# Performance work log

Hardware: AMD Instinct MI355X
Metric: run time of the kernel (lower is better)

Reference implementation:

```python
import math
import jax, jax.numpy as jnp
import numpy as np

B, N, M, H = 2, 4096, 32, 8
FDIM, LDIM, HID = 256, 10, 16
D = FDIM // H  # head_dim = 32


def setup_inputs() -> dict:
    key = jax.random.key(0)
    ks = jax.random.split(key, 16)
    rn = lambda i, shape, scale=1.0: jax.random.normal(ks[i], shape, jnp.float32) * scale
    return {
        "nbhd_pairwise_g": rn(0, (B, N, M, LDIM)),
        "nbhd_mask": jax.random.bernoulli(ks[1], 0.9, (B, N, M)),
        "key_features": rn(2, (B, N, FDIM)),
        "query_features": rn(3, (B, N, FDIM)),
        "nbhd_idx": jax.random.randint(ks[4], (B, N, M), 0, N, dtype=jnp.int32),
        # fc_k / fc_q (Linear feature_dim -> embed_dim)
        "Wk": rn(5, (FDIM, FDIM), 1.0 / math.sqrt(FDIM)),
        "bk": rn(6, (FDIM,), 0.01),
        "Wq": rn(7, (FDIM, FDIM), 1.0 / math.sqrt(FDIM)),
        "bq": rn(8, (FDIM,), 0.01),
        "W0": rn(9, (H, LDIM, HID), 1.0 / math.sqrt(LDIM)),
        "b0": rn(10, (H, HID), 0.01),
        "W1": rn(11, (H, HID, HID), 1.0 / math.sqrt(HID)),
        "b1": rn(12, (H, HID), 0.01),
        "W2": rn(13, (H, HID, 1), 1.0 / math.sqrt(HID)),
        "b2": rn(14, (H, 1), 0.01),
    }


def reference(nbhd_pairwise_g, nbhd_mask, key_features, query_features, nbhd_idx,
              Wk, bk, Wq, bq, W0, b0, W1, b1, W2, b2):
    # --- DotProductKernel: project, gather keys at nbhd_idx, scaled dot ---
    K = (key_features @ Wk + bk).reshape(B, N, H, D)      # (b,n,h,d)
    Q = (query_features @ Wq + bq).reshape(B, N, H, D)    # (b,n,h,d)
    # gather neighbor keys: Kn[b,i,j] = K[b, nbhd_idx[b,i,j]]  -> (b,n,m,h,d)
    Kn = K[jnp.arange(B)[:, None, None], nbhd_idx]
    # same math as full QK^T followed by A_[B,NNS,nbhd_idx], without the n x n matrix
    feat = jnp.einsum('bnhd,bnmhd->bnmh', Q, Kn) / math.sqrt(D)  # (b,n,m,h)

    # --- location featurisation: per-head MLP on pairwise group embedding ---
    h0 = jax.nn.silu(jnp.einsum('bnml,hlk->bnmhk', nbhd_pairwise_g, W0) + b0)
    h1 = jax.nn.silu(jnp.einsum('bnmhk,hkj->bnmhj', h0, W1) + b1)
    loc = jax.nn.silu(jnp.einsum('bnmhj,hjo->bnmho', h1, W2) + b2)[..., 0]  # (b,n,m,h)

    # --- combination 'sum' (both unsqueezed to 5D), normalisation 'none' ---
    out = (feat + loc)[..., None]  # (b,n,m,h,1)
    return out
```

## Files before the change

### kernel.cpp

```cpp
#include <hip/hip_runtime.h>

typedef unsigned int   u32;
typedef unsigned short u16;
typedef __bf16 bf16x8 __attribute__((ext_vector_type(8)));
typedef float  f32x4  __attribute__((ext_vector_type(4)));
typedef float  f32x16 __attribute__((ext_vector_type(16)));

__device__ __forceinline__ u16 f2b(float f) {
  u32 u = __float_as_uint(f);
  u = (u + 0x7fffu + ((u >> 16) & 1u)) >> 16;
  return (u16)u;
}
__device__ __forceinline__ float b2f_lo(u32 u) { return __uint_as_float(u << 16); }
__device__ __forceinline__ float b2f_hi(u32 u) { return __uint_as_float(u & 0xffff0000u); }
__device__ __forceinline__ float silu_f(float x) { return __fdividef(x, 1.f + __expf(-x)); }

__global__ void prep_wt(const float* __restrict__ Wk, const float* __restrict__ Wq,
                        u16* __restrict__ Wkt, u16* __restrict__ Wqt) {
  for (int idx = blockIdx.x * 256 + threadIdx.x; idx < 256 * 256; idx += gridDim.x * 256) {
    int n = idx >> 8, k = idx & 255;
    Wkt[idx] = f2b(Wk[k * 256 + n]);
    Wqt[idx] = f2b(Wq[k * 256 + n]);
  }
}

__global__ void prep_mlpfrag(const float* __restrict__ W0, const float* __restrict__ W1,
                             u16* __restrict__ W0A, u16* __restrict__ W1A) {
  int t = threadIdx.x;
  int h = t >> 6, l = t & 63;
  int hf = l >> 5, j = l & 31;
  #pragma unroll
  for (int e = 0; e < 8; e++) {
    int k = 8 * hf + e;
    float v0 = (j < 16 && k < 10) ? W0[h * 160 + k * 16 + j] : 0.f;
    W0A[t * 8 + e] = f2b(v0);
    int jin = (k & 3) + 8 * ((k >> 2) & 1) + 4 * (k >> 3);
    float v1 = (j < 16) ? W1[h * 256 + jin * 16 + j] : 0.f;
    W1A[t * 8 + e] = f2b(v1);
  }
}

#define LDA 72
__global__ __launch_bounds__(256) void gemm_proj(
    const float* __restrict__ A0, const float* __restrict__ A1,
    const u16* __restrict__ B0, const u16* __restrict__ B1,
    const float* __restrict__ bias0, const float* __restrict__ bias1,
    u16* __restrict__ C0, u16* __restrict__ C1) {
  const float* A; const u16* Bt; const float* bias; u16* C;
  if (blockIdx.z == 0) { A = A0; Bt = B0; bias = bias0; C = C0; }
  else                 { A = A1; Bt = B1; bias = bias1; C = C1; }
  __shared__ __align__(16) u16 As[128 * LDA];
  __shared__ __align__(16) u16 Bs[128 * LDA];
  const int t = threadIdx.x;
  const int w = t >> 6, lane = t & 63;
  const int wm = w >> 1, wn = w & 1;
  const int row0 = blockIdx.x * 128, col0 = blockIdx.y * 128;
  f32x4 acc[4][4] = {};
  for (int kk = 0; kk < 256; kk += 64) {
    #pragma unroll
    for (int p = 0; p < 8; p++) {
      int r = p * 16 + (t >> 4), q = (t & 15) * 4;
      float4 v = *(const float4*)(A + (size_t)(row0 + r) * 256 + kk + q);
      uint2 pk;
      pk.x = (u32)f2b(v.x) | ((u32)f2b(v.y) << 16);
      pk.y = (u32)f2b(v.z) | ((u32)f2b(v.w) << 16);
      *(uint2*)(&As[r * LDA + q]) = pk;
    }
    #pragma unroll
    for (int p = 0; p < 4; p++) {
      int r = p * 32 + (t >> 3), q = (t & 7) * 8;
      *(uint4*)(&Bs[r * LDA + q]) = *(const uint4*)(Bt + (size_t)(col0 + r) * 256 + kk + q);
    }
    __syncthreads();
    #pragma unroll
    for (int ks = 0; ks < 2; ks++) {
      bf16x8 af[4], bfr[4];
      #pragma unroll
      for (int i = 0; i < 4; i++) {
        af[i]  = *(const bf16x8*)(&As[(wm * 64 + i * 16 + (lane & 15)) * LDA + ks * 32 + (lane >> 4) * 8]);
        bfr[i] = *(const bf16x8*)(&Bs[(wn * 64 + i * 16 + (lane & 15)) * LDA + ks * 32 + (lane >> 4) * 8]);
      }
      #pragma unroll
      for (int i = 0; i < 4; i++)
        #pragma unroll
        for (int j = 0; j < 4; j++)
          acc[i][j] = __builtin_amdgcn_mfma_f32_16x16x32_bf16(af[i], bfr[j], acc[i][j], 0, 0, 0);
    }
    __syncthreads();
  }
  #pragma unroll
  for (int j = 0; j < 4; j++) {
    int c = col0 + wn * 64 + j * 16 + (lane & 15);
    float bv = bias[c];
    #pragma unroll
    for (int i = 0; i < 4; i++) {
      int r0 = row0 + wm * 64 + i * 16 + (lane >> 4) * 4;
      #pragma unroll
      for (int q = 0; q < 4; q++)
        C[(size_t)(r0 + q) * 256 + c] = f2b(acc[i][j][q] + bv);
    }
  }
}

__global__ __launch_bounds__(512) void fused_main(
    const u16* __restrict__ Kbf, const u16* __restrict__ Qbf,
    const int* __restrict__ nidx, const float* __restrict__ g,
    const u16* __restrict__ W0A, const u16* __restrict__ W1A,
    const float* __restrict__ b0, const float* __restrict__ b1,
    const float* __restrict__ W2, const float* __restrict__ b2,
    float* __restrict__ out) {
  __shared__ float lout[256];
  const int t = threadIdx.x;
  const int h = t >> 6, lane = t & 63;
  const int hf = lane >> 5, m = lane & 31;
  const int bn = blockIdx.x;
  const int b = bn >> 12;
  const int row = bn * 32 + m;
  const int hs = __builtin_amdgcn_readfirstlane(h);

  const bf16x8 a0 = *(const bf16x8*)(W0A + (size_t)(hs * 64 + lane) * 8);
  const bf16x8 a1 = *(const bf16x8*)(W1A + (size_t)(hs * 64 + lane) * 8);

  const float* gp = g + (size_t)row * 10;
  float2 v0 = *(const float2*)(gp + hf * 8);
  float2 v1, v2, v3;
  if (hf == 0) {
    v1 = *(const float2*)(gp + 2); v2 = *(const float2*)(gp + 4); v3 = *(const float2*)(gp + 6);
  } else {
    v1 = make_float2(0.f, 0.f); v2 = v1; v3 = v1;
  }
  bf16x8 gb;
  gb[0] = (__bf16)v0.x; gb[1] = (__bf16)v0.y;
  gb[2] = (__bf16)v1.x; gb[3] = (__bf16)v1.y;
  gb[4] = (__bf16)v2.x; gb[5] = (__bf16)v2.y;
  gb[6] = (__bf16)v3.x; gb[7] = (__bf16)v3.y;

  const int kidx = nidx[row];
  const size_t krow = (size_t)b * 4096 + (size_t)kidx;
  const uint4* qp = (const uint4*)(Qbf + (size_t)bn * 256 + h * 32 + hf * 16);
  const uint4* kp = (const uint4*)(Kbf + krow * 256 + h * 32 + hf * 16);
  uint4 q0 = qp[0], q1 = qp[1], k0 = kp[0], k1 = kp[1];
  float dpart = 0.f;
  dpart += b2f_lo(q0.x) * b2f_lo(k0.x) + b2f_hi(q0.x) * b2f_hi(k0.x);
  dpart += b2f_lo(q0.y) * b2f_lo(k0.y) + b2f_hi(q0.y) * b2f_hi(k0.y);
  dpart += b2f_lo(q0.z) * b2f_lo(k0.z) + b2f_hi(q0.z) * b2f_hi(k0.z);
  dpart += b2f_lo(q0.w) * b2f_lo(k0.w) + b2f_hi(q0.w) * b2f_hi(k0.w);
  dpart += b2f_lo(q1.x) * b2f_lo(k1.x) + b2f_hi(q1.x) * b2f_hi(k1.x);
  dpart += b2f_lo(q1.y) * b2f_lo(k1.y) + b2f_hi(q1.y) * b2f_hi(k1.y);
  dpart += b2f_lo(q1.z) * b2f_lo(k1.z) + b2f_hi(q1.z) * b2f_hi(k1.z);
  dpart += b2f_lo(q1.w) * b2f_lo(k1.w) + b2f_hi(q1.w) * b2f_hi(k1.w);

  const float* __restrict__ bb0 = b0 + hs * 16;
  const float* __restrict__ bb1 = b1 + hs * 16;
  const float* __restrict__ w2  = W2 + hs * 16;
  f32x16 zero = {};
  f32x16 acc0 = __builtin_amdgcn_mfma_f32_32x32x16_bf16(a0, gb, zero, 0, 0, 0);
  bf16x8 h0b;
  #pragma unroll
  for (int e = 0; e < 8; e++) {
    int c = (e & 3) + 8 * (e >> 2);
    float bj = hf ? bb0[c + 4] : bb0[c];
    h0b[e] = (__bf16)silu_f(acc0[e] + bj);
  }
  f32x16 acc1 = __builtin_amdgcn_mfma_f32_32x32x16_bf16(a1, h0b, zero, 0, 0, 0);
  float part = 0.f;
  #pragma unroll
  for (int e = 0; e < 8; e++) {
    int c = (e & 3) + 8 * (e >> 2);
    float bj = hf ? bb1[c + 4] : bb1[c];
    float wj = hf ? w2[c + 4] : w2[c];
    part += silu_f(acc1[e] + bj) * wj;
  }

  float osum = part + __shfl_xor(part, 32, 64);
  float feat = (dpart + __shfl_xor(dpart, 32, 64)) * 0.17677669529663687f;
  float res = feat + silu_f(osum + b2[hs]);

  if (hf == 0) lout[m * 8 + h] = res;
  __syncthreads();
  if (t < 64) {
    float4 v = ((const float4*)lout)[t];
    ((float4*)(out + (size_t)bn * 256))[t] = v;
  }
}

extern "C" void kernel_launch(void* const* d_in, const int* in_sizes, int n_in,
                              void* d_out, int out_size, void* d_ws, size_t ws_size,
                              hipStream_t stream) {
  const float* g_in = (const float*)d_in[0];
  const float* kf   = (const float*)d_in[2];
  const float* qf   = (const float*)d_in[3];
  const int*   idx  = (const int*)d_in[4];
  const float* Wk   = (const float*)d_in[5];
  const float* bk   = (const float*)d_in[6];
  const float* Wq   = (const float*)d_in[7];
  const float* bq   = (const float*)d_in[8];
  const float* W0   = (const float*)d_in[9];
  const float* b0   = (const float*)d_in[10];
  const float* W1   = (const float*)d_in[11];
  const float* b1   = (const float*)d_in[12];
  const float* W2   = (const float*)d_in[13];
  const float* b2   = (const float*)d_in[14];

  char* ws = (char*)d_ws;
  u16* Kbf = (u16*)ws;
  u16* Qbf = (u16*)(ws + 4u * 1024 * 1024);
  u16* Wkt = (u16*)(ws + 8u * 1024 * 1024);
  u16* Wqt = (u16*)(ws + 8u * 1024 * 1024 + 131072);
  u16* W0A = (u16*)(ws + 8u * 1024 * 1024 + 262144);
  u16* W1A = (u16*)(ws + 8u * 1024 * 1024 + 262144 + 8192);

  prep_wt<<<64, 256, 0, stream>>>(Wk, Wq, Wkt, Wqt);
  prep_mlpfrag<<<1, 512, 0, stream>>>(W0, W1, W0A, W1A);
  gemm_proj<<<dim3(64, 2, 2), 256, 0, stream>>>(kf, qf, Wkt, Wqt, bk, bq, Kbf, Qbf);
  fused_main<<<8192, 512, 0, stream>>>(Kbf, Qbf, idx, g_in, W0A, W1A, b0, b1, W2, b2,
                                       (float*)d_out);
}
```

Measured before the change: 76.49 us.

## Merge prep kernels, pre-lay out MLP biases, process two rows per block

```diff
diff --git a/kernel.cpp b/kernel.cpp
--- a/kernel.cpp
+++ b/kernel.cpp
@@ -15,28 +15,44 @@
 __device__ __forceinline__ float b2f_hi(u32 u) { return __uint_as_float(u & 0xffff0000u); }
 __device__ __forceinline__ float silu_f(float x) { return __fdividef(x, 1.f + __expf(-x)); }
 
-__global__ void prep_wt(const float* __restrict__ Wk, const float* __restrict__ Wq,
-                        u16* __restrict__ Wkt, u16* __restrict__ Wqt) {
-  for (int idx = blockIdx.x * 256 + threadIdx.x; idx < 256 * 256; idx += gridDim.x * 256) {
-    int n = idx >> 8, k = idx & 255;
-    Wkt[idx] = f2b(Wk[k * 256 + n]);
-    Wqt[idx] = f2b(Wq[k * 256 + n]);
-  }
-}
-
-__global__ void prep_mlpfrag(const float* __restrict__ W0, const float* __restrict__ W1,
-                             u16* __restrict__ W0A, u16* __restrict__ W1A) {
-  int t = threadIdx.x;
-  int h = t >> 6, l = t & 63;
-  int hf = l >> 5, j = l & 31;
-  #pragma unroll
-  for (int e = 0; e < 8; e++) {
-    int k = 8 * hf + e;
-    float v0 = (j < 16 && k < 10) ? W0[h * 160 + k * 16 + j] : 0.f;
-    W0A[t * 8 + e] = f2b(v0);
-    int jin = (k & 3) + 8 * ((k >> 2) & 1) + 4 * (k >> 3);
-    float v1 = (j < 16) ? W1[h * 256 + jin * 16 + j] : 0.f;
-    W1A[t * 8 + e] = f2b(v1);
+__device__ __forceinline__ float dot8(uint4 q, uint4 k, float acc) {
+  acc += b2f_lo(q.x) * b2f_lo(k.x) + b2f_hi(q.x) * b2f_hi(k.x);
+  acc += b2f_lo(q.y) * b2f_lo(k.y) + b2f_hi(q.y) * b2f_hi(k.y);
+  acc += b2f_lo(q.z) * b2f_lo(k.z) + b2f_hi(q.z) * b2f_hi(k.z);
+  acc += b2f_lo(q.w) * b2f_lo(k.w) + b2f_hi(q.w) * b2f_hi(k.w);
+  return acc;
+}
+
+__global__ __launch_bounds__(512) void prep_all(
+    const float* __restrict__ Wk, const float* __restrict__ Wq,
+    const float* __restrict__ W0, const float* __restrict__ W1,
+    const float* __restrict__ b0, const float* __restrict__ b1,
+    const float* __restrict__ W2,
+    u16* __restrict__ Wkt, u16* __restrict__ Wqt,
+    u16* __restrict__ W0A, u16* __restrict__ W1A, float* __restrict__ BT) {
+  const int blk = blockIdx.x, t = threadIdx.x;
+  if (blk < 64) {
+    for (int idx = blk * 512 + t; idx < 65536; idx += 64 * 512) {
+      int n = idx >> 8, k = idx & 255;
+      Wkt[idx] = f2b(Wk[k * 256 + n]);
+      Wqt[idx] = f2b(Wq[k * 256 + n]);
+    }
+  } else {
+    const int h = t >> 6, l = t & 63;
+    const int hf = l >> 5, j = l & 31;
+    #pragma unroll
+    for (int e = 0; e < 8; e++) {
+      int k = 8 * hf + e;
+      float v0 = (j < 16 && k < 10) ? W0[h * 160 + k * 16 + j] : 0.f;
+      W0A[t * 8 + e] = f2b(v0);
+      int jin = (k & 3) + 8 * ((k >> 2) & 1) + 4 * (k >> 3);
+      float v1 = (j < 16) ? W1[h * 256 + jin * 16 + j] : 0.f;
+      W1A[t * 8 + e] = f2b(v1);
+      int cj = (e & 3) + 8 * (e >> 2) + 4 * hf;
+      BT[t * 32 + e]      = b0[h * 16 + cj];
+      BT[t * 32 + 8 + e]  = b1[h * 16 + cj];
+      BT[t * 32 + 16 + e] = W2[h * 16 + cj];
+    }
   }
 }
 
@@ -106,81 +122,88 @@
     const u16* __restrict__ Kbf, const u16* __restrict__ Qbf,
     const int* __restrict__ nidx, const float* __restrict__ g,
     const u16* __restrict__ W0A, const u16* __restrict__ W1A,
-    const float* __restrict__ b0, const float* __restrict__ b1,
-    const float* __restrict__ W2, const float* __restrict__ b2,
+    const float* __restrict__ BT, const float* __restrict__ b2,
     float* __restrict__ out) {
-  __shared__ float lout[256];
+  __shared__ float lout[512];
   const int t = threadIdx.x;
   const int h = t >> 6, lane = t & 63;
   const int hf = lane >> 5, m = lane & 31;
-  const int bn = blockIdx.x;
-  const int b = bn >> 12;
-  const int row = bn * 32 + m;
+  const int bn0 = blockIdx.x * 2;
+  const int b = bn0 >> 12;
   const int hs = __builtin_amdgcn_readfirstlane(h);
 
   const bf16x8 a0 = *(const bf16x8*)(W0A + (size_t)(hs * 64 + lane) * 8);
   const bf16x8 a1 = *(const bf16x8*)(W1A + (size_t)(hs * 64 + lane) * 8);
-
-  const float* gp = g + (size_t)row * 10;
-  float2 v0 = *(const float2*)(gp + hf * 8);
-  float2 v1, v2, v3;
+  const float4* btp = (const float4*)(BT + (size_t)t * 32);
+  const float4 t0 = btp[0], t1 = btp[1], t2 = btp[2], t3 = btp[3], t4 = btp[4], t5 = btp[5];
+  const float bj0[8] = {t0.x, t0.y, t0.z, t0.w, t1.x, t1.y, t1.z, t1.w};
+  const float bj1[8] = {t2.x, t2.y, t2.z, t2.w, t3.x, t3.y, t3.z, t3.w};
+  const float wj[8]  = {t4.x, t4.y, t4.z, t4.w, t5.x, t5.y, t5.z, t5.w};
+  const float b2s = b2[hs];
+
+  const int row0 = bn0 * 32 + m;
+  const int i0 = nidx[row0], i1 = nidx[row0 + 32];
+
+  const float* gp0 = g + (size_t)row0 * 10;
+  const float* gp1 = gp0 + 320;
+  float2 gA0 = *(const float2*)(gp0 + hf * 8);
+  float2 gB0 = *(const float2*)(gp1 + hf * 8);
+  float2 gA1 = {0.f, 0.f}, gA2 = gA1, gA3 = gA1, gB1 = gA1, gB2 = gA1, gB3 = gA1;
   if (hf == 0) {
-    v1 = *(const float2*)(gp + 2); v2 = *(const float2*)(gp + 4); v3 = *(const float2*)(gp + 6);
-  } else {
-    v1 = make_float2(0.f, 0.f); v2 = v1; v3 = v1;
-  }
-  bf16x8 gb;
-  gb[0] = (__bf16)v0.x; gb[1] = (__bf16)v0.y;
-  gb[2] = (__bf16)v1.x; gb[3] = (__bf16)v1.y;
-  gb[4] = (__bf16)v2.x; gb[5] = (__bf16)v2.y;
-  gb[6] = (__bf16)v3.x; gb[7] = (__bf16)v3.y;
-
-  const int kidx = nidx[row];
-  const size_t krow = (size_t)b * 4096 + (size_t)kidx;
-  const uint4* qp = (const uint4*)(Qbf + (size_t)bn * 256 + h * 32 + hf * 16);
-  const uint4* kp = (const uint4*)(Kbf + krow * 256 + h * 32 + hf * 16);
-  uint4 q0 = qp[0], q1 = qp[1], k0 = kp[0], k1 = kp[1];
-  float dpart = 0.f;
-  dpart += b2f_lo(q0.x) * b2f_lo(k0.x) + b2f_hi(q0.x) * b2f_hi(k0.x);
-  dpart += b2f_lo(q0.y) * b2f_lo(k0.y) + b2f_hi(q0.y) * b2f_hi(k0.y);
-  dpart += b2f_lo(q0.z) * b2f_lo(k0.z) + b2f_hi(q0.z) * b2f_hi(k0.z);
-  dpart += b2f_lo(q0.w) * b2f_lo(k0.w) + b2f_hi(q0.w) * b2f_hi(k0.w);
-  dpart += b2f_lo(q1.x) * b2f_lo(k1.x) + b2f_hi(q1.x) * b2f_hi(k1.x);
-  dpart += b2f_lo(q1.y) * b2f_lo(k1.y) + b2f_hi(q1.y) * b2f_hi(k1.y);
-  dpart += b2f_lo(q1.z) * b2f_lo(k1.z) + b2f_hi(q1.z) * b2f_hi(k1.z);
-  dpart += b2f_lo(q1.w) * b2f_lo(k1.w) + b2f_hi(q1.w) * b2f_hi(k1.w);
-
-  const float* __restrict__ bb0 = b0 + hs * 16;
-  const float* __restrict__ bb1 = b1 + hs * 16;
-  const float* __restrict__ w2  = W2 + hs * 16;
-  f32x16 zero = {};
-  f32x16 acc0 = __builtin_amdgcn_mfma_f32_32x32x16_bf16(a0, gb, zero, 0, 0, 0);
+    gA1 = *(const float2*)(gp0 + 2); gA2 = *(const float2*)(gp0 + 4); gA3 = *(const float2*)(gp0 + 6);
+    gB1 = *(const float2*)(gp1 + 2); gB2 = *(const float2*)(gp1 + 4); gB3 = *(const float2*)(gp1 + 6);
+  }
+
+  const uint4* qp0 = (const uint4*)(Qbf + (size_t)bn0 * 256 + h * 32 + hf * 16);
+  const uint4* qp1 = (const uint4*)(Qbf + (size_t)(bn0 + 1) * 256 + h * 32 + hf * 16);
+  const uint4* kp0 = (const uint4*)(Kbf + ((size_t)b * 4096 + i0) * 256 + h * 32 + hf * 16);
+  const uint4* kp1 = (const uint4*)(Kbf + ((size_t)b * 4096 + i1) * 256 + h * 32 + hf * 16);
+  uint4 qA0 = qp0[0], qA1 = qp0[1], kA0 = kp0[0], kA1 = kp0[1];
+  uint4 qB0 = qp1[0], qB1 = qp1[1], kB0 = kp1[0], kB1 = kp1[1];
+
+  float d0 = dot8(qA1, kA1, dot8(qA0, kA0, 0.f));
+  float d1 = dot8(qB1, kB1, dot8(qB0, kB0, 0.f));
+
+  bf16x8 gf0, gf1;
+  gf0[0] = (__bf16)gA0.x; gf0[1] = (__bf16)gA0.y; gf0[2] = (__bf16)gA1.x; gf0[3] = (__bf16)gA1.y;
+  gf0[4] = (__bf16)gA2.x; gf0[5] = (__bf16)gA2.y; gf0[6] = (__bf16)gA3.x; gf0[7] = (__bf16)gA3.y;
+  gf1[0] = (__bf16)gB0.x; gf1[1] = (__bf16)gB0.y; gf1[2] = (__bf16)gB1.x; gf1[3] = (__bf16)gB1.y;
+  gf1[4] = (__bf16)gB2.x; gf1[5] = (__bf16)gB2.y; gf1[6] = (__bf16)gB3.x; gf1[7] = (__bf16)gB3.y;
+
+  const f32x16 z = {};
+
+  f32x16 acc = __builtin_amdgcn_mfma_f32_32x32x16_bf16(a0, gf0, z, 0, 0, 0);
   bf16x8 h0b;
   #pragma unroll
-  for (int e = 0; e < 8; e++) {
-    int c = (e & 3) + 8 * (e >> 2);
-    float bj = hf ? bb0[c + 4] : bb0[c];
-    h0b[e] = (__bf16)silu_f(acc0[e] + bj);
-  }
-  f32x16 acc1 = __builtin_amdgcn_mfma_f32_32x32x16_bf16(a1, h0b, zero, 0, 0, 0);
-  float part = 0.f;
-  #pragma unroll
-  for (int e = 0; e < 8; e++) {
-    int c = (e & 3) + 8 * (e >> 2);
-    float bj = hf ? bb1[c + 4] : bb1[c];
-    float wj = hf ? w2[c + 4] : w2[c];
-    part += silu_f(acc1[e] + bj) * wj;
-  }
-
-  float osum = part + __shfl_xor(part, 32, 64);
-  float feat = (dpart + __shfl_xor(dpart, 32, 64)) * 0.17677669529663687f;
-  float res = feat + silu_f(osum + b2[hs]);
-
-  if (hf == 0) lout[m * 8 + h] = res;
+  for (int e = 0; e < 8; e++) h0b[e] = (__bf16)silu_f(acc[e] + bj0[e]);
+  acc = __builtin_amdgcn_mfma_f32_32x32x16_bf16(a1, h0b, z, 0, 0, 0);
+  float p0 = 0.f;
+  #pragma unroll
+  for (int e = 0; e < 8; e++) p0 += silu_f(acc[e] + bj1[e]) * wj[e];
+
+  acc = __builtin_amdgcn_mfma_f32_32x32x16_bf16(a0, gf1, z, 0, 0, 0);
+  #pragma unroll
+  for (int e = 0; e < 8; e++) h0b[e] = (__bf16)silu_f(acc[e] + bj0[e]);
+  acc = __builtin_amdgcn_mfma_f32_32x32x16_bf16(a1, h0b, z, 0, 0, 0);
+  float p1 = 0.f;
+  #pragma unroll
+  for (int e = 0; e < 8; e++) p1 += silu_f(acc[e] + bj1[e]) * wj[e];
+
+  float o0 = p0 + __shfl_xor(p0, 32, 64);
+  float o1 = p1 + __shfl_xor(p1, 32, 64);
+  float f0 = (d0 + __shfl_xor(d0, 32, 64)) * 0.17677669529663687f;
+  float f1 = (d1 + __shfl_xor(d1, 32, 64)) * 0.17677669529663687f;
+  float res0 = f0 + silu_f(o0 + b2s);
+  float res1 = f1 + silu_f(o1 + b2s);
+
+  if (hf == 0) {
+    lout[m * 8 + h]       = res0;
+    lout[256 + m * 8 + h] = res1;
+  }
   __syncthreads();
-  if (t < 64) {
+  if (t < 128) {
     float4 v = ((const float4*)lout)[t];
-    ((float4*)(out + (size_t)bn * 256))[t] = v;
+    ((float4*)(out + (size_t)bn0 * 256))[t] = v;
   }
 }
 
@@ -203,16 +226,16 @@
   const float* b2   = (const float*)d_in[14];
 
   char* ws = (char*)d_ws;
-  u16* Kbf = (u16*)ws;
-  u16* Qbf = (u16*)(ws + 4u * 1024 * 1024);
-  u16* Wkt = (u16*)(ws + 8u * 1024 * 1024);
-  u16* Wqt = (u16*)(ws + 8u * 1024 * 1024 + 131072);
-  u16* W0A = (u16*)(ws + 8u * 1024 * 1024 + 262144);
-  u16* W1A = (u16*)(ws + 8u * 1024 * 1024 + 262144 + 8192);
-
-  prep_wt<<<64, 256, 0, stream>>>(Wk, Wq, Wkt, Wqt);
-  prep_mlpfrag<<<1, 512, 0, stream>>>(W0, W1, W0A, W1A);
+  u16*   Kbf = (u16*)ws;
+  u16*   Qbf = (u16*)(ws + 4u * 1024 * 1024);
+  u16*   Wkt = (u16*)(ws + 8u * 1024 * 1024);
+  u16*   Wqt = (u16*)(ws + 8u * 1024 * 1024 + 131072);
+  u16*   W0A = (u16*)(ws + 8u * 1024 * 1024 + 262144);
+  u16*   W1A = (u16*)(ws + 8u * 1024 * 1024 + 262144 + 8192);
+  float* BT  = (float*)(ws + 8u * 1024 * 1024 + 262144 + 16384);
+
+  prep_all<<<65, 512, 0, stream>>>(Wk, Wq, W0, W1, b0, b1, W2, Wkt, Wqt, W0A, W1A, BT);
   gemm_proj<<<dim3(64, 2, 2), 256, 0, stream>>>(kf, qf, Wkt, Wqt, bk, bq, Kbf, Qbf);
-  fused_main<<<8192, 512, 0, stream>>>(Kbf, Qbf, idx, g_in, W0A, W1A, b0, b1, W2, b2,
+  fused_main<<<4096, 512, 0, stream>>>(Kbf, Qbf, idx, g_in, W0A, W1A, BT, b2,
                                        (float*)d_out);
 }
```

Result: slower. 84.66 us (+10.7%).
